# Optimization experiments

Hardware: AMD Instinct MI355X
Metric: run time of the kernel (lower is better)

Reference implementation:

```python
import jax, jax.numpy as jnp
import numpy as np

B, T, F, H, S = 32, 2000, 80, 256, 100
CH = [256, 256]
D = 2 * H  # bidirectional output dim


def _conv1d_relu(x, w, b):
    # x: (B,C_in,T), w: (C_out,C_in,3), 'same' padding, eval-mode dropout = identity
    y = jax.lax.conv_general_dilated(x, w, (1,), [(1, 1)], dimension_numbers=("NCH", "OIH", "NCH"))
    return jax.nn.relu(y + b[None, :, None])


def _lstm_dir(x, mask, wih, whh, b):
    # Masked LSTM == packed-sequence semantics: state frozen and output zero past length.
    # PyTorch gate order: i, f, g, o.  x: (B,T,I), mask: (B,T) bool
    Bb = x.shape[0]
    Hh = whh.shape[1]
    h0 = jnp.zeros((Bb, Hh), x.dtype)

    def step(carry, inp):
        h, c = carry
        xt, mt = inp
        g = xt @ wih.T + h @ whh.T + b
        i, f, gg, o = jnp.split(g, 4, axis=-1)
        i = jax.nn.sigmoid(i)
        f = jax.nn.sigmoid(f)
        gg = jnp.tanh(gg)
        o = jax.nn.sigmoid(o)
        cn = f * c + i * gg
        hn = o * jnp.tanh(cn)
        m = mt[:, None]
        return (jnp.where(m, hn, h), jnp.where(m, cn, c)), jnp.where(m, hn, 0.0)

    _, ys = jax.lax.scan(step, (h0, h0), (jnp.swapaxes(x, 0, 1), jnp.swapaxes(mask, 0, 1)))
    return jnp.swapaxes(ys, 0, 1)  # (B,T,H)


def _bilstm_layer(x, mask, lengths, wih, whh, b):
    fwd = _lstm_dir(x, mask, wih[0], whh[0], b[0])
    t = jnp.arange(x.shape[1])[None, :]
    # reverse each sequence within its valid prefix (involution), identity on padding
    rev_idx = jnp.where(t < lengths[:, None], lengths[:, None] - 1 - t, t)
    x_rev = jnp.take_along_axis(x, rev_idx[:, :, None], axis=1)
    bwd = _lstm_dir(x_rev, mask, wih[1], whh[1], b[1])
    bwd = jnp.take_along_axis(bwd, rev_idx[:, :, None], axis=1)
    return jnp.concatenate([fwd, bwd], axis=-1)


def _head(x, w1, b1, w2, b2):
    # Linear -> ReLU -> (Dropout=id) -> Linear(.,1), squeeze last dim
    return (jax.nn.relu(x @ w1.T + b1) @ w2.T + b2)[..., 0]


def _forward(features, feat_lengths, phoneme_segments, seg_lengths,
             conv1_w, conv1_b, conv2_w, conv2_b,
             wih0, whh0, bias0, wih1, whh1, bias1,
             seg_w1, seg_b1, seg_w2, seg_b2,
             utt_w1, utt_b1, utt_w2, utt_b2):
    x = jnp.swapaxes(features, 1, 2)  # (B,F,T)
    x = _conv1d_relu(x, conv1_w, conv1_b)
    x = _conv1d_relu(x, conv2_w, conv2_b)
    x = jnp.swapaxes(x, 1, 2)  # (B,T,C)

    t = jnp.arange(x.shape[1])[None, :]
    mask = t < feat_lengths[:, None]  # (B,T)

    h = _bilstm_layer(x, mask, feat_lengths, wih0, whh0, bias0)
    lstm_out = _bilstm_layer(h, mask, feat_lengths, wih1, whh1, bias1)  # (B,T,2H), zeros at pads

    denom = jnp.maximum(feat_lengths, 1).astype(lstm_out.dtype)[:, None]
    pooled = lstm_out.sum(axis=1) / denom
    utterance_score = _head(pooled, utt_w1, utt_b1, utt_w2, utt_b2)  # (B,)

    # vectorized segment mean-pool (replaces the python double loop)
    s = jnp.clip(phoneme_segments[..., 0], 0, feat_lengths[:, None])
    e = jnp.maximum(s + 1, jnp.minimum(phoneme_segments[..., 1], feat_lengths[:, None]))
    seg_mask = (t[:, None, :] >= s[..., None]) & (t[:, None, :] < e[..., None])  # (B,S,T)
    counts = (e - s).astype(lstm_out.dtype)
    seg_mean = jnp.einsum("bst,btd->bsd", seg_mask.astype(lstm_out.dtype), lstm_out) / counts[..., None]
    scores = _head(seg_mean, seg_w1, seg_b1, seg_w2, seg_b2)  # (B,S)
    valid = jnp.arange(scores.shape[1])[None, :] < seg_lengths[:, None]
    phoneme_scores = jnp.where(valid, scores, 0.0)
    return utterance_score, phoneme_scores


def setup_inputs() -> dict:
    key = jax.random.key(0)
    ks = jax.random.split(key, 24)
    sc = 0.05
    features = jax.random.normal(ks[0], (B, T, F), jnp.float32)
    feat_lengths = jax.random.randint(ks[1], (B,), T // 2, T + 1, dtype=jnp.int32)
    sidx = jnp.arange(S, dtype=jnp.int32)
    starts = (feat_lengths[:, None] * sidx) // S
    ends = (feat_lengths[:, None] * (sidx + 1)) // S
    phoneme_segments = jnp.stack([starts, ends], axis=-1).astype(jnp.int32)  # (B,S,2)
    seg_lengths = jnp.full((B,), S, dtype=jnp.int32)
    return {
        "features": features,
        "feat_lengths": feat_lengths,
        "phoneme_segments": phoneme_segments,
        "seg_lengths": seg_lengths,
        "conv1_w": jax.random.normal(ks[2], (CH[0], F, 3), jnp.float32) * sc,
        "conv1_b": jnp.zeros((CH[0],), jnp.float32),
        "conv2_w": jax.random.normal(ks[3], (CH[1], CH[0], 3), jnp.float32) * sc,
        "conv2_b": jnp.zeros((CH[1],), jnp.float32),
        "wih0": jax.random.normal(ks[4], (2, 4 * H, CH[1]), jnp.float32) * sc,
        "whh0": jax.random.normal(ks[5], (2, 4 * H, H), jnp.float32) * sc,
        "bias0": jnp.zeros((2, 4 * H), jnp.float32),
        "wih1": jax.random.normal(ks[6], (2, 4 * H, 2 * H), jnp.float32) * sc,
        "whh1": jax.random.normal(ks[7], (2, 4 * H, H), jnp.float32) * sc,
        "bias1": jnp.zeros((2, 4 * H), jnp.float32),
        "seg_w1": jax.random.normal(ks[8], (D, D), jnp.float32) * sc,
        "seg_b1": jnp.zeros((D,), jnp.float32),
        "seg_w2": jax.random.normal(ks[9], (1, D), jnp.float32) * sc,
        "seg_b2": jnp.zeros((1,), jnp.float32),
        "utt_w1": jax.random.normal(ks[10], (D, D), jnp.float32) * sc,
        "utt_b1": jnp.zeros((D,), jnp.float32),
        "utt_w2": jax.random.normal(ks[11], (1, D), jnp.float32) * sc,
        "utt_b2": jnp.zeros((1,), jnp.float32),
    }


def reference(features, feat_lengths, phoneme_segments, seg_lengths,
              conv1_w, conv1_b, conv2_w, conv2_b,
              wih0, whh0, bias0, wih1, whh1, bias1,
              seg_w1, seg_b1, seg_w2, seg_b2,
              utt_w1, utt_b1, utt_w2, utt_b2):
    return _forward(features, feat_lengths, phoneme_segments, seg_lengths,
                    conv1_w, conv1_b, conv2_w, conv2_b,
                    wih0, whh0, bias0, wih1, whh1, bias1,
                    seg_w1, seg_b1, seg_w2, seg_b2,
                    utt_w1, utt_b1, utt_w2, utt_b2)
```

## Files before the change

kernel.cpp:

```cpp
#include <hip/hip_runtime.h>
#include <math.h>

#define T_SEQ 2000
#define BATCH 32
#define NSEG  100

typedef unsigned short bf16_t;
typedef unsigned int   u32;
typedef _Float16       half_t;
typedef half_t half2_t __attribute__((ext_vector_type(2)));

#define KP_REG 96
#define KP_LDS 32
#define NG     (KP_LDS / 4)

__device__ __forceinline__ float sigmoidf_(float x) {
    return 1.0f / (1.0f + __expf(-x));
}
__device__ __forceinline__ float tanh_(float x) {
    return 1.0f - 2.0f / (__expf(2.0f * x) + 1.0f);
}
__device__ __forceinline__ float bf2f(bf16_t u) {
    return __uint_as_float((unsigned)u << 16);
}
__device__ __forceinline__ bf16_t f2bf(float f) {
    unsigned x = __float_as_uint(f);
    return (bf16_t)((x + 0x7FFFu + ((x >> 16) & 1u)) >> 16);
}
__device__ __forceinline__ u32 f2h(float f) {
    return (u32)__builtin_bit_cast(unsigned short, (half_t)f);
}
__device__ __forceinline__ float dot2f(u32 w, u32 h, float acc) {
    return __builtin_amdgcn_fdot2(__builtin_bit_cast(half2_t, w),
                                  __builtin_bit_cast(half2_t, h), acc, false);
}
__device__ __forceinline__ u32 rl(u32 v, int l) {
    return (u32)__builtin_amdgcn_readlane((int)v, l);
}

__device__ __forceinline__ float4 ld4(const float* p) { return *(const float4*)p; }
__device__ __forceinline__ float4 ld4(const bf16_t* p) {
    ushort4 u = *(const ushort4*)p;
    return make_float4(bf2f(u.x), bf2f(u.y), bf2f(u.z), bf2f(u.w));
}

__global__ void ws_guard_kernel(float* out, int n) {
    int i = blockIdx.x * blockDim.x + threadIdx.x;
    if (i < n) out[i] = 1e30f;
}

__global__ void transpose3(const float* __restrict__ in, float* __restrict__ out,
                           int D0, int D1, int D2) {
    int i = blockIdx.x * blockDim.x + threadIdx.x;
    int tot = D0 * D1 * D2;
    if (i >= tot) return;
    int d0 = i / (D1 * D2);
    int r  = i - d0 * (D1 * D2);
    int d1 = r / D2;
    int d2 = r - d1 * D2;
    out[(size_t)d0 * D1 * D2 + (size_t)d2 * D1 + d1] = in[i];
}

__global__ __launch_bounds__(256) void pack_whh(const float* __restrict__ whhT,
                                                u32* __restrict__ w16,
                                                u32* __restrict__ wp4) {
    int i = blockIdx.x * 256 + threadIdx.x;
    int d  = i >> 17;
    int r  = i & 131071;
    int kp = r >> 10;
    int j  = r & 1023;
    const float* base = whhT + (size_t)d * 262144;
    u32 lo = f2h(base[(size_t)(2 * kp)     * 1024 + j]);
    u32 hi = f2h(base[(size_t)(2 * kp + 1) * 1024 + j]);
    u32 val = lo | (hi << 16);
    w16[i] = val;
    if (kp >= KP_REG) {
        int g  = (kp - KP_REG) >> 2;
        int cc = (kp - KP_REG) & 3;
        size_t idx = ((((size_t)d * 2 + (j & 1)) * NG + g) * 512 + (j >> 1)) * 4 + cc;
        wp4[idx] = val;
    }
}

template <int MODE, int CIN, typename TA, bool OUT_BF>
__global__ __launch_bounds__(256) void gemm_nt(
    const TA* __restrict__ A, const float* __restrict__ W,
    const float* __restrict__ bias, void* __restrict__ Cout,
    void* __restrict__ Cout2,
    int M, int N, int K, int relu, int t0, int chunkM,
    const int* __restrict__ lens)
{
    __shared__ u32 As[16 * 258];
    __shared__ u32 Ws[16 * 66];
    const int tid    = threadIdx.x;
    const int m_base = blockIdx.x * 256;
    const int n_base = blockIdx.y * 64;
    const int m0     = (tid >> 3) * 8;
    const int n0     = (tid & 7) * 8;
    int zrev = 0;
    if constexpr (MODE == 4) {
        zrev = blockIdx.z;
        if (zrev) { W += (size_t)N * K; bias += N; Cout = Cout2; }
    }
    float acc[8][8] = {};

    for (int k0 = 0; k0 < K; k0 += 32) {
#pragma unroll
        for (int i = 0; i < 8; ++i) {
            int f4  = i * 256 + tid;
            int row = f4 >> 3;
            int k4  = (f4 & 7) << 2;
            int gm  = m_base + row;
            int gk  = k0 + k4;
            float4 v = make_float4(0.f, 0.f, 0.f, 0.f);
            if (gm < M && gk < K) {
                if constexpr (MODE == 1) {
                    int bb  = gm / T_SEQ;
                    int tt  = gm - bb * T_SEQ;
                    int tap = gk / CIN;
                    int cc  = gk - tap * CIN;
                    int ts  = tt + tap - 1;
                    if (ts >= 0 && ts < T_SEQ)
                        v = ld4(A + ((size_t)(bb * T_SEQ + ts) * CIN + cc));
                } else {
                    int bb = gm / chunkM;
                    int r  = gm - bb * chunkM;
                    int t;
                    if constexpr (MODE == 2)      t = t0 + r;
                    else if constexpr (MODE == 3) t = lens[bb] - 1 - (t0 + r);
                    else t = zrev ? (lens[bb] - 1 - (t0 + r)) : (t0 + r);
                    if (t >= 0 && t < T_SEQ)
                        v = ld4(A + ((size_t)(bb * T_SEQ + t) * K + gk));
                }
            }
            int kp = k4 >> 1;
            As[(kp + 0) * 258 + row] = f2h(v.x) | (f2h(v.y) << 16);
            As[(kp + 1) * 258 + row] = f2h(v.z) | (f2h(v.w) << 16);
        }
#pragma unroll
        for (int i = 0; i < 2; ++i) {
            int f4  = i * 256 + tid;
            int row = f4 >> 3;
            int k4  = (f4 & 7) << 2;
            int gn  = n_base + row;
            int gk  = k0 + k4;
            float4 v = make_float4(0.f, 0.f, 0.f, 0.f);
            if (gk < K)
                v = *(const float4*)(W + (size_t)gn * K + gk);
            int kp = k4 >> 1;
            Ws[(kp + 0) * 66 + row] = f2h(v.x) | (f2h(v.y) << 16);
            Ws[(kp + 1) * 66 + row] = f2h(v.z) | (f2h(v.w) << 16);
        }
        __syncthreads();
#pragma unroll 8
        for (int kk = 0; kk < 16; ++kk) {
            u32 am[8], wn[8];
#pragma unroll
            for (int j = 0; j < 4; ++j) {
                uint2 a = *(const uint2*)(As + kk * 258 + m0 + 2 * j);
                am[2 * j] = a.x; am[2 * j + 1] = a.y;
                uint2 w = *(const uint2*)(Ws + kk * 66 + n0 + 2 * j);
                wn[2 * j] = w.x; wn[2 * j + 1] = w.y;
            }
#pragma unroll
            for (int im = 0; im < 8; ++im)
#pragma unroll
                for (int in = 0; in < 8; ++in)
                    acc[im][in] = dot2f(am[im], wn[in], acc[im][in]);
        }
        __syncthreads();
    }

    float bs[8];
#pragma unroll
    for (int j = 0; j < 8; ++j) bs[j] = bias[n_base + n0 + j];
#pragma unroll
    for (int im = 0; im < 8; ++im) {
        int gm = m_base + m0 + im;
        if (gm < M) {
            float o[8];
#pragma unroll
            for (int j = 0; j < 8; ++j) {
                float v = acc[im][j] + bs[j];
                o[j] = relu ? fmaxf(v, 0.f) : v;
            }
            if constexpr (OUT_BF) {
                bf16_t* crow = (bf16_t*)Cout + (size_t)gm * N + n_base + n0;
                ushort4 u0 = { f2bf(o[0]), f2bf(o[1]), f2bf(o[2]), f2bf(o[3]) };
                ushort4 u1 = { f2bf(o[4]), f2bf(o[5]), f2bf(o[6]), f2bf(o[7]) };
                *(ushort4*)(crow)     = u0;
                *(ushort4*)(crow + 4) = u1;
            } else {
                float* crow = (float*)Cout + (size_t)gm * N + n_base + n0;
                *(float4*)(crow)     = make_float4(o[0], o[1], o[2], o[3]);
                *(float4*)(crow + 4) = make_float4(o[4], o[5], o[6], o[7]);
            }
        }
    }
}

__global__
__attribute__((amdgpu_flat_work_group_size(512, 512), amdgpu_waves_per_eu(2, 2)))
void lstm_rec_phase(
    const float* __restrict__ XpF, const float* __restrict__ XpB,
    const u32* __restrict__ whh16, const uint4* __restrict__ wp4,
    const int* __restrict__ lens,
    float* __restrict__ state, bf16_t* __restrict__ Hout, int s0, int chunk)
{
    __shared__ __align__(16) uint4 wlds4[2 * NG * 512];
    __shared__ __align__(16) float gs[1024];
    __shared__ __align__(16) u32   hp[128];

    const int bd   = blockIdx.x;
    const int b    = bd >> 1;
    const int d    = bd & 1;
    const int t    = threadIdx.x;
    const int j0   = t * 2;
    const int lane = t & 63;
    const int len  = lens[b];
    const int s1   = min(s0 + chunk, len);
    const u32*   Wg = whh16 + (size_t)d * (128 * 1024);
    const uint4* Wp = wp4   + (size_t)d * (2 * NG * 512);

    uint2 w2[KP_REG];
#pragma unroll
    for (int kp = 0; kp < KP_REG; ++kp)
        w2[kp] = *(const uint2*)(Wg + (size_t)kp * 1024 + j0);
#pragma unroll
    for (int i = 0; i < 2 * NG; ++i)
        wlds4[i * 512 + t] = Wp[i * 512 + t];

    float* st = state + bd * 512;
    float c = 0.f, hcur = 0.f;
    if (t < 256) {
        if (s0 > 0) { hcur = st[t]; c = st[256 + t]; }
        u32 hb = f2h(hcur);
        u32 ob = (u32)__shfl_xor((int)hb, 1);
        if (!(t & 1)) hp[t >> 1] = hb | (ob << 16);
    }
    __syncthreads();

    const float* xrow = ((d ? XpB : XpF) + (size_t)b * ((size_t)chunk * 1024));
    const uint4* wpA = wlds4 + t;
    const uint4* wpB = wlds4 + NG * 512 + t;
    for (int s = s0; s < s1; ++s, xrow += 1024) {
        float2 xv = *(const float2*)(xrow + j0);
        uint2 hreg = *(const uint2*)(hp + 2 * lane);
        float a0 = 0.f, a1 = 0.f, b0 = 0.f, b1 = 0.f;
#pragma unroll
        for (int kp = 0; kp < KP_REG; kp += 2) {
            u32 h0 = rl(hreg.x, kp >> 1);
            u32 h1 = rl(hreg.y, kp >> 1);
            a0 = dot2f(w2[kp].x,     h0, a0); a1 = dot2f(w2[kp].y,     h0, a1);
            b0 = dot2f(w2[kp + 1].x, h1, b0); b1 = dot2f(w2[kp + 1].y, h1, b1);
        }
#pragma unroll
        for (int g = 0; g < NG; ++g) {
            uint4 wA = wpA[g * 512];
            uint4 wB = wpB[g * 512];
            const int lb = (KP_REG >> 1) + 2 * g;
            u32 h0 = rl(hreg.x, lb);
            u32 h1 = rl(hreg.y, lb);
            u32 h2 = rl(hreg.x, lb + 1);
            u32 h3 = rl(hreg.y, lb + 1);
            a0 = dot2f(wA.x, h0, a0); a1 = dot2f(wB.x, h0, a1);
            b0 = dot2f(wA.y, h1, b0); b1 = dot2f(wB.y, h1, b1);
            a0 = dot2f(wA.z, h2, a0); a1 = dot2f(wB.z, h2, a1);
            b0 = dot2f(wA.w, h3, b0); b1 = dot2f(wB.w, h3, b1);
        }
        *(float2*)(gs + j0) = make_float2(a0 + b0 + xv.x, a1 + b1 + xv.y);
        __syncthreads();
        if (t < 256) {
            float ig = sigmoidf_(gs[t]);
            float fg = sigmoidf_(gs[256 + t]);
            float gg = tanh_(gs[512 + t]);
            float og = sigmoidf_(gs[768 + t]);
            c = fmaf(fg, c, ig * gg);
            float hn = og * tanh_(c);
            const int tau = d ? (len - 1 - s) : s;
            Hout[(size_t)(b * T_SEQ + tau) * 512 + (d << 8) + t] = f2bf(hn);
            u32 hb = f2h(hn);
            u32 ob = (u32)__shfl_xor((int)hb, 1);
            if (!(t & 1)) hp[t >> 1] = hb | (ob << 16);
            hcur = hn;
        }
        __syncthreads();
    }
    if (t < 256) { st[t] = hcur; st[256 + t] = c; }
}

__global__ __launch_bounds__(256) void pooled_kernel(
    const bf16_t* __restrict__ L, const int* __restrict__ lens,
    float* __restrict__ pooled)
{
    const int b     = blockIdx.x;
    const int chunk = blockIdx.y;
    const int tid   = threadIdx.x;
    const int len   = lens[b];
    const int t0    = chunk * 250;
    const int t1    = min(t0 + 250, len);
    const float inv = 1.f / fmaxf((float)len, 1.f);
    float s0 = 0.f, s1 = 0.f;
    for (int t = t0; t < t1; ++t) {
        const bf16_t* row = L + (size_t)(b * T_SEQ + t) * 512;
        s0 += bf2f(row[tid]);
        s1 += bf2f(row[tid + 256]);
    }
    if (t1 > t0) {
        atomicAdd(&pooled[b * 512 + tid], s0 * inv);
        atomicAdd(&pooled[b * 512 + 256 + tid], s1 * inv);
    }
}

__global__ __launch_bounds__(256) void utt_head(
    const float* __restrict__ pooled,
    const float* __restrict__ w1T, const float* __restrict__ b1,
    const float* __restrict__ w2, const float* __restrict__ b2,
    float* __restrict__ out)
{
    const int b   = blockIdx.x;
    const int tid = threadIdx.x;
    __shared__ float p[512];
    __shared__ float hid[512];
    __shared__ float red[4];
    p[tid]       = pooled[b * 512 + tid];
    p[tid + 256] = pooled[b * 512 + 256 + tid];
    __syncthreads();
#pragma unroll
    for (int half = 0; half < 2; ++half) {
        int u = tid + half * 256;
        float a = b1[u];
#pragma unroll 8
        for (int k = 0; k < 512; ++k) a = fmaf(w1T[(size_t)k * 512 + u], p[k], a);
        hid[u] = fmaxf(a, 0.f);
    }
    __syncthreads();
    float part = hid[tid] * w2[tid] + hid[tid + 256] * w2[tid + 256];
    for (int off = 32; off; off >>= 1) part += __shfl_down(part, off, 64);
    if ((tid & 63) == 0) red[tid >> 6] = part;
    __syncthreads();
    if (tid == 0) out[b] = red[0] + red[1] + red[2] + red[3] + b2[0];
}

__global__ __launch_bounds__(256) void seg_head(
    const bf16_t* __restrict__ L, const int* __restrict__ lens,
    const int* __restrict__ segs,
    const float* __restrict__ w1T, const float* __restrict__ b1,
    const float* __restrict__ w2, const float* __restrict__ b2,
    const int* __restrict__ seg_lens, float* __restrict__ out)
{
    const int blk = blockIdx.x;
    const int b   = blk / NSEG;
    const int s   = blk - b * NSEG;
    const int tid = threadIdx.x;
    __shared__ float m[512];
    __shared__ float hid[512];
    __shared__ float red[4];
    const int len = lens[b];
    int st = segs[blk * 2 + 0];
    int en = segs[blk * 2 + 1];
    st = min(max(st, 0), len);
    en = max(st + 1, min(en, len));
    const float inv = 1.f / (float)(en - st);
    float a0 = 0.f, a1 = 0.f;
    for (int t = st; t < en; ++t) {
        const bf16_t* row = L + (size_t)(b * T_SEQ + t) * 512;
        a0 += bf2f(row[tid]);
        a1 += bf2f(row[tid + 256]);
    }
    m[tid]       = a0 * inv;
    m[tid + 256] = a1 * inv;
    __syncthreads();
#pragma unroll
    for (int half = 0; half < 2; ++half) {
        int u = tid + half * 256;
        float a = b1[u];
#pragma unroll 8
        for (int k = 0; k < 512; ++k) a = fmaf(w1T[(size_t)k * 512 + u], m[k], a);
        hid[u] = fmaxf(a, 0.f);
    }
    __syncthreads();
    float part = hid[tid] * w2[tid] + hid[tid + 256] * w2[tid + 256];
    for (int off = 32; off; off >>= 1) part += __shfl_down(part, off, 64);
    if ((tid & 63) == 0) red[tid >> 6] = part;
    __syncthreads();
    if (tid == 0)
        out[BATCH + blk] = (s < seg_lens[b]) ? red[0] + red[1] + red[2] + red[3] + b2[0]
                                             : 0.f;
}

extern "C" void kernel_launch(void* const* d_in, const int* in_sizes, int n_in,
                              void* d_out, int out_size, void* d_ws, size_t ws_size,
                              hipStream_t stream)
{
    const float* features = (const float*)d_in[0];
    const int*   feat_len = (const int*)d_in[1];
    const int*   segs     = (const int*)d_in[2];
    const int*   seg_lens = (const int*)d_in[3];
    const float* conv1_w  = (const float*)d_in[4];
    const float* conv1_b  = (const float*)d_in[5];
    const float* conv2_w  = (const float*)d_in[6];
    const float* conv2_b  = (const float*)d_in[7];
    const float* wih0     = (const float*)d_in[8];
    const float* whh0     = (const float*)d_in[9];
    const float* bias0    = (const float*)d_in[10];
    const float* wih1     = (const float*)d_in[11];
    const float* whh1     = (const float*)d_in[12];
    const float* bias1    = (const float*)d_in[13];
    const float* seg_w1   = (const float*)d_in[14];
    const float* seg_b1   = (const float*)d_in[15];
    const float* seg_w2   = (const float*)d_in[16];
    const float* seg_b2   = (const float*)d_in[17];
    const float* utt_w1   = (const float*)d_in[18];
    const float* utt_b1   = (const float*)d_in[19];
    const float* utt_w2   = (const float*)d_in[20];
    const float* utt_b2   = (const float*)d_in[21];
    float* out = (float*)d_out;
    char*  wsb = (char*)d_ws;

    size_t off = 0;
    auto alloc = [&](size_t bytes) -> size_t {
        size_t o = off;
        off += (bytes + 255) & ~(size_t)255;
        return o;
    };
    const size_t o_wt1    = alloc(61440  * 4);
    const size_t o_wt2    = alloc(196608 * 4);
    const size_t o_whh0T  = alloc(524288 * 4);
    const size_t o_whh1T  = alloc(524288 * 4);
    const size_t o_w16_0  = alloc(262144 * 4);
    const size_t o_w16_1  = alloc(262144 * 4);
    const size_t o_wp4_0  = alloc((size_t)2 * 2 * NG * 512 * 16);
    const size_t o_wp4_1  = alloc((size_t)2 * 2 * NG * 512 * 16);
    const size_t o_sw1T   = alloc(262144 * 4);
    const size_t o_uw1T   = alloc(262144 * 4);
    const size_t o_state  = alloc(32768  * 4);
    const size_t o_pooled = alloc(16384  * 4);
    const size_t o_Hcat   = alloc((size_t)32768000 * 2);
    const size_t o_lstm   = alloc((size_t)32768000 * 2);
    const size_t o_y1     = o_lstm;
    const size_t o_x2     = o_lstm + (size_t)16384000 * 2;
    const size_t fixed_end = off;

    const int cands[] = {250, 200, 125, 100, 50, 40, 25, 20, 10};
    int chunk = 0;
    size_t o_XpF = 0, o_XpB = 0;
    for (int ci = 0; ci < 9; ++ci) {
        int c = cands[ci];
        size_t xp_bytes = ((size_t)c * 32 * 1024 * 4 + 255) & ~(size_t)255;
        if (fixed_end + 2 * xp_bytes <= ws_size) {
            chunk = c;
            o_XpF = fixed_end;
            o_XpB = fixed_end + xp_bytes;
            break;
        }
    }
    if (chunk == 0) {
        ws_guard_kernel<<<(out_size + 255) / 256, 256, 0, stream>>>(out, out_size);
        return;
    }
    const int nph = T_SEQ / chunk;

    float*  wt1    = (float*)(wsb + o_wt1);
    float*  wt2    = (float*)(wsb + o_wt2);
    float*  whh0T  = (float*)(wsb + o_whh0T);
    float*  whh1T  = (float*)(wsb + o_whh1T);
    u32*    w16_0  = (u32*)(wsb + o_w16_0);
    u32*    w16_1  = (u32*)(wsb + o_w16_1);
    u32*    wp4_0  = (u32*)(wsb + o_wp4_0);
    u32*    wp4_1  = (u32*)(wsb + o_wp4_1);
    float*  sw1T   = (float*)(wsb + o_sw1T);
    float*  uw1T   = (float*)(wsb + o_uw1T);
    float*  state  = (float*)(wsb + o_state);
    float*  pooled = (float*)(wsb + o_pooled);
    bf16_t* Hcat   = (bf16_t*)(wsb + o_Hcat);
    bf16_t* lstm   = (bf16_t*)(wsb + o_lstm);
    bf16_t* y1     = (bf16_t*)(wsb + o_y1);
    bf16_t* x2     = (bf16_t*)(wsb + o_x2);
    float*  XpF    = (float*)(wsb + o_XpF);
    float*  XpB    = (float*)(wsb + o_XpB);

    hipMemsetAsync(state, 0, 32768 * 4, stream);
    hipMemsetAsync(pooled, 0, 16384 * 4, stream);

    transpose3<<<240, 256, 0, stream>>>(conv1_w, wt1, 256, 80, 3);
    transpose3<<<768, 256, 0, stream>>>(conv2_w, wt2, 256, 256, 3);
    transpose3<<<2048, 256, 0, stream>>>(whh0, whh0T, 2, 1024, 256);
    transpose3<<<2048, 256, 0, stream>>>(whh1, whh1T, 2, 1024, 256);
    transpose3<<<1024, 256, 0, stream>>>(seg_w1, sw1T, 1, 512, 512);
    transpose3<<<1024, 256, 0, stream>>>(utt_w1, uw1T, 1, 512, 512);
    pack_whh<<<1024, 256, 0, stream>>>(whh0T, w16_0, wp4_0);
    pack_whh<<<1024, 256, 0, stream>>>(whh1T, w16_1, wp4_1);

    gemm_nt<1, 80, float, true><<<dim3(250, 4), 256, 0, stream>>>(
        features, wt1, conv1_b, y1, nullptr, 64000, 256, 240, 1, 0, 0, feat_len);
    gemm_nt<1, 256, bf16_t, true><<<dim3(250, 4), 256, 0, stream>>>(
        y1, wt2, conv2_b, x2, nullptr, 64000, 256, 768, 1, 0, 0, feat_len);

    const int gx = (32 * chunk + 255) / 256;
    const int Mc = 32 * chunk;

    for (int p = 0; p < nph; ++p) {
        const int t0 = p * chunk;
        gemm_nt<4, 1, bf16_t, false><<<dim3(gx, 16, 2), 256, 0, stream>>>(
            x2, wih0, bias0, XpF, XpB, Mc, 1024, 256, 0, t0, chunk, feat_len);
        lstm_rec_phase<<<64, 512, 0, stream>>>(
            XpF, XpB, w16_0, (const uint4*)wp4_0, feat_len, state, Hcat, t0, chunk);
    }

    hipMemsetAsync(state, 0, 32768 * 4, stream);

    for (int p = 0; p < nph; ++p) {
        const int t0 = p * chunk;
        gemm_nt<4, 1, bf16_t, false><<<dim3(gx, 16, 2), 256, 0, stream>>>(
            Hcat, wih1, bias1, XpF, XpB, Mc, 1024, 512, 0, t0, chunk, feat_len);
        lstm_rec_phase<<<64, 512, 0, stream>>>(
            XpF, XpB, w16_1, (const uint4*)wp4_1, feat_len, state, lstm, t0, chunk);
    }

    pooled_kernel<<<dim3(32, 8), 256, 0, stream>>>(lstm, feat_len, pooled);
    utt_head<<<32, 256, 0, stream>>>(pooled, uw1T, utt_b1, utt_w2, utt_b2, out);

    seg_head<<<3200, 256, 0, stream>>>(lstm, feat_len, segs, sw1T, seg_b1,
                                       seg_w2, seg_b2, seg_lens, out);
}
```

Baseline: 10.77 ms.

## Overlap next chunk's input-projection GEMM with LSTM recurrence in one fused kernel

Merges the per-chunk input-projection GEMM into the recurrence kernel. Blocks 0-63 run the serial LSTM recurrence for the current chunk while the remaining 192 blocks compute the projection for the next chunk into a second, double-buffered Xp buffer. This is meant to hide the GEMM and its launch behind the latency-bound recurrence instead of serializing them. In exchange it needs twice the Xp workspace, which may force a smaller chunk size and more phases, and the GEMM blocks may contend with the recurrence blocks for memory bandwidth.

```diff
diff --git a/kernel.cpp b/kernel.cpp
--- a/kernel.cpp
+++ b/kernel.cpp
@@ -125,10 +125,7 @@
                 } else {
                     int bb = gm / chunkM;
                     int r  = gm - bb * chunkM;
-                    int t;
-                    if constexpr (MODE == 2)      t = t0 + r;
-                    else if constexpr (MODE == 3) t = lens[bb] - 1 - (t0 + r);
-                    else t = zrev ? (lens[bb] - 1 - (t0 + r)) : (t0 + r);
+                    int t  = zrev ? (lens[bb] - 1 - (t0 + r)) : (t0 + r);
                     if (t >= 0 && t < T_SEQ)
                         v = ld4(A + ((size_t)(bb * T_SEQ + t) * K + gk));
                 }
@@ -201,92 +198,198 @@
 
 __global__
 __attribute__((amdgpu_flat_work_group_size(512, 512), amdgpu_waves_per_eu(2, 2)))
-void lstm_rec_phase(
+void rec_fused(
     const float* __restrict__ XpF, const float* __restrict__ XpB,
     const u32* __restrict__ whh16, const uint4* __restrict__ wp4,
     const int* __restrict__ lens,
-    float* __restrict__ state, bf16_t* __restrict__ Hout, int s0, int chunk)
+    float* __restrict__ state, bf16_t* __restrict__ Hout, int s0, int chunk,
+    const bf16_t* __restrict__ Ag, const float* __restrict__ Wg2,
+    const float* __restrict__ biasg, float* __restrict__ XpFn,
+    float* __restrict__ XpBn, int Kg, int t0n)
 {
-    __shared__ __align__(16) uint4 wlds4[2 * NG * 512];
-    __shared__ __align__(16) float gs[1024];
-    __shared__ __align__(16) u32   hp[128];
-
-    const int bd   = blockIdx.x;
-    const int b    = bd >> 1;
-    const int d    = bd & 1;
-    const int t    = threadIdx.x;
-    const int j0   = t * 2;
-    const int lane = t & 63;
-    const int len  = lens[b];
-    const int s1   = min(s0 + chunk, len);
-    const u32*   Wg = whh16 + (size_t)d * (128 * 1024);
-    const uint4* Wp = wp4   + (size_t)d * (2 * NG * 512);
-
-    uint2 w2[KP_REG];
-#pragma unroll
-    for (int kp = 0; kp < KP_REG; ++kp)
-        w2[kp] = *(const uint2*)(Wg + (size_t)kp * 1024 + j0);
-#pragma unroll
-    for (int i = 0; i < 2 * NG; ++i)
-        wlds4[i * 512 + t] = Wp[i * 512 + t];
-
-    float* st = state + bd * 512;
-    float c = 0.f, hcur = 0.f;
-    if (t < 256) {
-        if (s0 > 0) { hcur = st[t]; c = st[256 + t]; }
-        u32 hb = f2h(hcur);
-        u32 ob = (u32)__shfl_xor((int)hb, 1);
-        if (!(t & 1)) hp[t >> 1] = hb | (ob << 16);
-    }
-    __syncthreads();
-
-    const float* xrow = ((d ? XpB : XpF) + (size_t)b * ((size_t)chunk * 1024));
-    const uint4* wpA = wlds4 + t;
-    const uint4* wpB = wlds4 + NG * 512 + t;
-    for (int s = s0; s < s1; ++s, xrow += 1024) {
-        float2 xv = *(const float2*)(xrow + j0);
-        uint2 hreg = *(const uint2*)(hp + 2 * lane);
-        float a0 = 0.f, a1 = 0.f, b0 = 0.f, b1 = 0.f;
-#pragma unroll
-        for (int kp = 0; kp < KP_REG; kp += 2) {
-            u32 h0 = rl(hreg.x, kp >> 1);
-            u32 h1 = rl(hreg.y, kp >> 1);
-            a0 = dot2f(w2[kp].x,     h0, a0); a1 = dot2f(w2[kp].y,     h0, a1);
-            b0 = dot2f(w2[kp + 1].x, h1, b0); b1 = dot2f(w2[kp + 1].y, h1, b1);
-        }
-#pragma unroll
-        for (int g = 0; g < NG; ++g) {
-            uint4 wA = wpA[g * 512];
-            uint4 wB = wpB[g * 512];
-            const int lb = (KP_REG >> 1) + 2 * g;
-            u32 h0 = rl(hreg.x, lb);
-            u32 h1 = rl(hreg.y, lb);
-            u32 h2 = rl(hreg.x, lb + 1);
-            u32 h3 = rl(hreg.y, lb + 1);
-            a0 = dot2f(wA.x, h0, a0); a1 = dot2f(wB.x, h0, a1);
-            b0 = dot2f(wA.y, h1, b0); b1 = dot2f(wB.y, h1, b1);
-            a0 = dot2f(wA.z, h2, a0); a1 = dot2f(wB.z, h2, a1);
-            b0 = dot2f(wA.w, h3, b0); b1 = dot2f(wB.w, h3, b1);
-        }
-        *(float2*)(gs + j0) = make_float2(a0 + b0 + xv.x, a1 + b1 + xv.y);
-        __syncthreads();
+    __shared__ __align__(16) u32 smem[32768 + 1024 + 128];
+
+    const int t = threadIdx.x;
+
+    if (blockIdx.x < 64) {
+        uint4* wlds4 = (uint4*)smem;
+        float* gs    = (float*)(smem + 32768);
+        u32*   hp    = smem + 32768 + 1024;
+
+        const int bd   = blockIdx.x;
+        const int b    = bd >> 1;
+        const int d    = bd & 1;
+        const int j0   = t * 2;
+        const int lane = t & 63;
+        const int len  = lens[b];
+        const int s1   = min(s0 + chunk, len);
+        const u32*   Wg = whh16 + (size_t)d * (128 * 1024);
+        const uint4* Wp = wp4   + (size_t)d * (2 * NG * 512);
+
+        uint2 w2[KP_REG];
+#pragma unroll
+        for (int kp = 0; kp < KP_REG; ++kp)
+            w2[kp] = *(const uint2*)(Wg + (size_t)kp * 1024 + j0);
+#pragma unroll
+        for (int i = 0; i < 2 * NG; ++i)
+            wlds4[i * 512 + t] = Wp[i * 512 + t];
+
+        float* st = state + bd * 512;
+        float c = 0.f, hcur = 0.f;
         if (t < 256) {
-            float ig = sigmoidf_(gs[t]);
-            float fg = sigmoidf_(gs[256 + t]);
-            float gg = tanh_(gs[512 + t]);
-            float og = sigmoidf_(gs[768 + t]);
-            c = fmaf(fg, c, ig * gg);
-            float hn = og * tanh_(c);
-            const int tau = d ? (len - 1 - s) : s;
-            Hout[(size_t)(b * T_SEQ + tau) * 512 + (d << 8) + t] = f2bf(hn);
-            u32 hb = f2h(hn);
+            if (s0 > 0) { hcur = st[t]; c = st[256 + t]; }
+            u32 hb = f2h(hcur);
             u32 ob = (u32)__shfl_xor((int)hb, 1);
             if (!(t & 1)) hp[t >> 1] = hb | (ob << 16);
-            hcur = hn;
         }
         __syncthreads();
-    }
-    if (t < 256) { st[t] = hcur; st[256 + t] = c; }
+
+        const float* xrow = ((d ? XpB : XpF) + (size_t)b * ((size_t)chunk * 1024));
+        const uint4* wpA = wlds4 + t;
+        const uint4* wpB = wlds4 + NG * 512 + t;
+        for (int s = s0; s < s1; ++s, xrow += 1024) {
+            float2 xv = *(const float2*)(xrow + j0);
+            uint2 hreg = *(const uint2*)(hp + 2 * lane);
+            float a0 = 0.f, a1 = 0.f, b0 = 0.f, b1 = 0.f;
+#pragma unroll
+            for (int kp = 0; kp < KP_REG; kp += 2) {
+                u32 h0 = rl(hreg.x, kp >> 1);
+                u32 h1 = rl(hreg.y, kp >> 1);
+                a0 = dot2f(w2[kp].x,     h0, a0); a1 = dot2f(w2[kp].y,     h0, a1);
+                b0 = dot2f(w2[kp + 1].x, h1, b0); b1 = dot2f(w2[kp + 1].y, h1, b1);
+            }
+#pragma unroll
+            for (int g = 0; g < NG; ++g) {
+                uint4 wA = wpA[g * 512];
+                uint4 wB = wpB[g * 512];
+                const int lb = (KP_REG >> 1) + 2 * g;
+                u32 h0 = rl(hreg.x, lb);
+                u32 h1 = rl(hreg.y, lb);
+                u32 h2 = rl(hreg.x, lb + 1);
+                u32 h3 = rl(hreg.y, lb + 1);
+                a0 = dot2f(wA.x, h0, a0); a1 = dot2f(wB.x, h0, a1);
+                b0 = dot2f(wA.y, h1, b0); b1 = dot2f(wB.y, h1, b1);
+                a0 = dot2f(wA.z, h2, a0); a1 = dot2f(wB.z, h2, a1);
+                b0 = dot2f(wA.w, h3, b0); b1 = dot2f(wB.w, h3, b1);
+            }
+            *(float2*)(gs + j0) = make_float2(a0 + b0 + xv.x, a1 + b1 + xv.y);
+            __syncthreads();
+            if (t < 256) {
+                float ig = sigmoidf_(gs[t]);
+                float fg = sigmoidf_(gs[256 + t]);
+                float gg = tanh_(gs[512 + t]);
+                float og = sigmoidf_(gs[768 + t]);
+                c = fmaf(fg, c, ig * gg);
+                float hn = og * tanh_(c);
+                const int tau = d ? (len - 1 - s) : s;
+                Hout[(size_t)(b * T_SEQ + tau) * 512 + (d << 8) + t] = f2bf(hn);
+                u32 hb = f2h(hn);
+                u32 ob = (u32)__shfl_xor((int)hb, 1);
+                if (!(t & 1)) hp[t >> 1] = hb | (ob << 16);
+                hcur = hn;
+            }
+            __syncthreads();
+        }
+        if (t < 256) { st[t] = hcur; st[256 + t] = c; }
+        return;
+    }
+
+    if (t0n < 0) return;
+    const int ngb = gridDim.x - 64;
+    const int gb  = blockIdx.x - 64;
+    u32* As  = smem;
+    u32* Ws0 = smem + 4128;
+    u32* Ws1 = smem + 4128 + 1056;
+    const int half = t >> 8;
+    const int ltid = t & 255;
+    u32* Wsh = half ? Ws1 : Ws0;
+    const int m0  = (ltid >> 3) * 8;
+    const int n0l = (ltid & 7) * 8;
+    const int Mc  = 32 * chunk;
+    const int gxm = (Mc + 255) >> 8;
+    const int U   = gxm * 8 * 2;
+
+    for (int u = gb; u < U; u += ngb) {
+        const int dir  = u & 1;
+        const int rem  = u >> 1;
+        const int mt   = rem >> 3;
+        const int np   = rem & 7;
+        const int m_base = mt * 256;
+        const int n_base = np * 128 + half * 64;
+        const float* Wd = Wg2 + (size_t)dir * (1024 * (size_t)Kg);
+        const float* bd = biasg + dir * 1024;
+        float* Xout = dir ? XpBn : XpFn;
+        float acc[8][8] = {};
+
+        for (int k0 = 0; k0 < Kg; k0 += 32) {
+#pragma unroll
+            for (int i = 0; i < 4; ++i) {
+                int f4  = i * 512 + t;
+                int row = f4 >> 3;
+                int k4  = (f4 & 7) << 2;
+                int gm  = m_base + row;
+                int gk  = k0 + k4;
+                float4 v = make_float4(0.f, 0.f, 0.f, 0.f);
+                if (gm < Mc && gk < Kg) {
+                    int bb = gm / chunk;
+                    int rr = gm - bb * chunk;
+                    int tt = dir ? (lens[bb] - 1 - (t0n + rr)) : (t0n + rr);
+                    if (tt >= 0 && tt < T_SEQ)
+                        v = ld4(Ag + ((size_t)(bb * T_SEQ + tt) * Kg + gk));
+                }
+                int kp = k4 >> 1;
+                As[(kp + 0) * 258 + row] = f2h(v.x) | (f2h(v.y) << 16);
+                As[(kp + 1) * 258 + row] = f2h(v.z) | (f2h(v.w) << 16);
+            }
+#pragma unroll
+            for (int i = 0; i < 2; ++i) {
+                int f4  = i * 256 + ltid;
+                int row = f4 >> 3;
+                int k4  = (f4 & 7) << 2;
+                int gn  = n_base + row;
+                int gk  = k0 + k4;
+                float4 v = make_float4(0.f, 0.f, 0.f, 0.f);
+                if (gk < Kg)
+                    v = *(const float4*)(Wd + (size_t)gn * Kg + gk);
+                int kp = k4 >> 1;
+                Wsh[(kp + 0) * 66 + row] = f2h(v.x) | (f2h(v.y) << 16);
+                Wsh[(kp + 1) * 66 + row] = f2h(v.z) | (f2h(v.w) << 16);
+            }
+            __syncthreads();
+#pragma unroll 8
+            for (int kk = 0; kk < 16; ++kk) {
+                u32 am[8], wn[8];
+#pragma unroll
+                for (int j = 0; j < 4; ++j) {
+                    uint2 a = *(const uint2*)(As + kk * 258 + m0 + 2 * j);
+                    am[2 * j] = a.x; am[2 * j + 1] = a.y;
+                    uint2 w = *(const uint2*)(Wsh + kk * 66 + n0l + 2 * j);
+                    wn[2 * j] = w.x; wn[2 * j + 1] = w.y;
+                }
+#pragma unroll
+                for (int im = 0; im < 8; ++im)
+#pragma unroll
+                    for (int in = 0; in < 8; ++in)
+                        acc[im][in] = dot2f(am[im], wn[in], acc[im][in]);
+            }
+            __syncthreads();
+        }
+
+        float bs[8];
+#pragma unroll
+        for (int j = 0; j < 8; ++j) bs[j] = bd[n_base + n0l + j];
+#pragma unroll
+        for (int im = 0; im < 8; ++im) {
+            int gm = m_base + m0 + im;
+            if (gm < Mc) {
+                float* crow = Xout + (size_t)gm * 1024 + n_base + n0l;
+                *(float4*)(crow)     = make_float4(acc[im][0] + bs[0], acc[im][1] + bs[1],
+                                                   acc[im][2] + bs[2], acc[im][3] + bs[3]);
+                *(float4*)(crow + 4) = make_float4(acc[im][4] + bs[4], acc[im][5] + bs[5],
+                                                   acc[im][6] + bs[6], acc[im][7] + bs[7]);
+            }
+        }
+    }
 }
 
 __global__ __launch_bounds__(256) void pooled_kernel(
@@ -444,14 +547,16 @@
 
     const int cands[] = {250, 200, 125, 100, 50, 40, 25, 20, 10};
     int chunk = 0;
-    size_t o_XpF = 0, o_XpB = 0;
+    size_t o_Xp[2][2] = {};
     for (int ci = 0; ci < 9; ++ci) {
         int c = cands[ci];
         size_t xp_bytes = ((size_t)c * 32 * 1024 * 4 + 255) & ~(size_t)255;
-        if (fixed_end + 2 * xp_bytes <= ws_size) {
+        if (fixed_end + 4 * xp_bytes <= ws_size) {
             chunk = c;
-            o_XpF = fixed_end;
-            o_XpB = fixed_end + xp_bytes;
+            o_Xp[0][0] = fixed_end;
+            o_Xp[0][1] = fixed_end + xp_bytes;
+            o_Xp[1][0] = fixed_end + 2 * xp_bytes;
+            o_Xp[1][1] = fixed_end + 3 * xp_bytes;
             break;
         }
     }
@@ -477,8 +582,8 @@
     bf16_t* lstm   = (bf16_t*)(wsb + o_lstm);
     bf16_t* y1     = (bf16_t*)(wsb + o_y1);
     bf16_t* x2     = (bf16_t*)(wsb + o_x2);
-    float*  XpF    = (float*)(wsb + o_XpF);
-    float*  XpB    = (float*)(wsb + o_XpB);
+    float*  XpF[2] = { (float*)(wsb + o_Xp[0][0]), (float*)(wsb + o_Xp[1][0]) };
+    float*  XpB[2] = { (float*)(wsb + o_Xp[0][1]), (float*)(wsb + o_Xp[1][1]) };
 
     hipMemsetAsync(state, 0, 32768 * 4, stream);
     hipMemsetAsync(pooled, 0, 16384 * 4, stream);
@@ -500,22 +605,26 @@
     const int gx = (32 * chunk + 255) / 256;
     const int Mc = 32 * chunk;
 
+    gemm_nt<4, 1, bf16_t, false><<<dim3(gx, 16, 2), 256, 0, stream>>>(
+        x2, wih0, bias0, XpF[0], XpB[0], Mc, 1024, 256, 0, 0, chunk, feat_len);
     for (int p = 0; p < nph; ++p) {
-        const int t0 = p * chunk;
-        gemm_nt<4, 1, bf16_t, false><<<dim3(gx, 16, 2), 256, 0, stream>>>(
-            x2, wih0, bias0, XpF, XpB, Mc, 1024, 256, 0, t0, chunk, feat_len);
-        lstm_rec_phase<<<64, 512, 0, stream>>>(
-            XpF, XpB, w16_0, (const uint4*)wp4_0, feat_len, state, Hcat, t0, chunk);
+        const int t0n = (p + 1 < nph) ? (p + 1) * chunk : -1;
+        rec_fused<<<256, 512, 0, stream>>>(
+            XpF[p & 1], XpB[p & 1], w16_0, (const uint4*)wp4_0, feat_len,
+            state, Hcat, p * chunk, chunk,
+            x2, wih0, bias0, XpF[(p + 1) & 1], XpB[(p + 1) & 1], 256, t0n);
     }
 
     hipMemsetAsync(state, 0, 32768 * 4, stream);
 
+    gemm_nt<4, 1, bf16_t, false><<<dim3(gx, 16, 2), 256, 0, stream>>>(
+        Hcat, wih1, bias1, XpF[0], XpB[0], Mc, 1024, 512, 0, 0, chunk, feat_len);
     for (int p = 0; p < nph; ++p) {
-        const int t0 = p * chunk;
-        gemm_nt<4, 1, bf16_t, false><<<dim3(gx, 16, 2), 256, 0, stream>>>(
-            Hcat, wih1, bias1, XpF, XpB, Mc, 1024, 512, 0, t0, chunk, feat_len);
-        lstm_rec_phase<<<64, 512, 0, stream>>>(
-            XpF, XpB, w16_1, (const uint4*)wp4_1, feat_len, state, lstm, t0, chunk);
+        const int t0n = (p + 1 < nph) ? (p + 1) * chunk : -1;
+        rec_fused<<<256, 512, 0, stream>>>(
+            XpF[p & 1], XpB[p & 1], w16_1, (const uint4*)wp4_1, feat_len,
+            state, lstm, p * chunk, chunk,
+            Hcat, wih1, bias1, XpF[(p + 1) & 1], XpB[(p + 1) & 1], 512, t0n);
     }
 
     pooled_kernel<<<dim3(32, 8), 256, 0, stream>>>(lstm, feat_len, pooled);
```

New measurement: 8.625 ms. -19.9%, faster.
